# Kernel optimization log

Measured on AMD Instinct MI355X. Metric: run time of the kernel, lower is better.

The kernel has to match this reference:

```python
import jax, jax.numpy as jnp
import numpy as np

N, E, D, DE, H = 50000, 400000, 128, 64, 8
EPS = 1e-5
SLOPE = 0.2


def setup_inputs() -> dict:
    key = jax.random.key(0)
    ks = jax.random.split(key, 16)

    def lin(k, fan_in, fan_out):
        return (jax.random.normal(k, (fan_in, fan_out), jnp.float32) / np.sqrt(fan_in)).astype(jnp.float32)

    return {
        "node_features": jax.random.normal(ks[0], (N, D), jnp.float32),
        "edge_features": jax.random.normal(ks[1], (E, DE), jnp.float32),
        "Wn": lin(ks[2], D, D), "bn": jnp.zeros((D,), jnp.float32),
        "Wq": lin(ks[3], D, D), "bq": jnp.zeros((D,), jnp.float32),
        "Wk": lin(ks[4], D, D), "bk": jnp.zeros((D,), jnp.float32),
        "Wv": lin(ks[5], D, D), "bv": jnp.zeros((D,), jnp.float32),
        "We": lin(ks[6], DE, D), "be": jnp.zeros((D,), jnp.float32),
        "A1": lin(ks[7], 3 * D, D), "b1": jnp.zeros((D,), jnp.float32),
        "A2": lin(ks[8], D, H), "b2": jnp.zeros((H,), jnp.float32),
        "gamma": jnp.ones((D,), jnp.float32),
        "beta": jnp.zeros((D,), jnp.float32),
        "edge_index": jax.random.randint(ks[9], (2, E), 0, N, dtype=jnp.int32),
    }


def reference(node_features, edge_features, Wn, bn, Wq, bq, Wk, bk, Wv, bv,
              We, be, A1, b1, A2, b2, gamma, beta, edge_index):
    num_nodes = node_features.shape[0]
    h = node_features @ Wn + bn                      # [N, D]
    q = node_features @ Wq + bq                      # [N, D]
    k = node_features @ Wk + bk                      # [N, D]
    v = node_features @ Wv + bv                      # [N, D]
    eh = edge_features @ We + be                     # [E, D]

    src, tgt = edge_index[0], edge_index[1]
    attn_in = jnp.concatenate([q[src], k[tgt], eh], axis=-1)   # [E, 3D]
    hmid = jax.nn.leaky_relu(attn_in @ A1 + b1, SLOPE)          # [E, D]
    scores = jax.nn.leaky_relu(hmid @ A2 + b2, SLOPE)           # [E, H]
    w = jax.nn.softmax(scores.mean(axis=-1), axis=0)            # global softmax over edges, [E]

    # scatter-add: output[src] += w * v[tgt]
    out = jax.ops.segment_sum(w[:, None] * v[tgt], src, num_segments=num_nodes)  # [N, D]

    y = h + out                                       # dropout = identity (eval)
    mu = y.mean(axis=-1, keepdims=True)
    var = y.var(axis=-1, keepdims=True)
    return gamma * (y - mu) / jnp.sqrt(var + EPS) + beta
```

## Files before the change

kernel.cpp:

```cpp
#include <hip/hip_runtime.h>

#define D 128
#define DE 64
#define SLOPE 0.2f
#define EPS 1e-5f

typedef float f32x4 __attribute__((ext_vector_type(4)));
typedef short bf16x8 __attribute__((ext_vector_type(8)));
typedef unsigned short ushort;

__device__ __forceinline__ float lrelu(float x) { return x > 0.f ? x : SLOPE * x; }

__device__ __forceinline__ ushort f2bf(float x) {
  union { float f; unsigned u; } c; c.f = x;
  unsigned r = c.u + 0x7FFFu + ((c.u >> 16) & 1u);
  return (ushort)(r >> 16);
}
__device__ __forceinline__ float bf2f(unsigned u) {
  return __uint_as_float(u << 16);
}
__device__ __forceinline__ uint4 cvt8(const float* p) {
  float4 f0 = *(const float4*)p;
  float4 f1 = *(const float4*)(p + 4);
  union { ushort us[8]; uint4 v; } u;
  u.us[0] = f2bf(f0.x); u.us[1] = f2bf(f0.y);
  u.us[2] = f2bf(f0.z); u.us[3] = f2bf(f0.w);
  u.us[4] = f2bf(f1.x); u.us[5] = f2bf(f1.y);
  u.us[6] = f2bf(f1.z); u.us[7] = f2bf(f1.w);
  return u.v;
}

__global__ __launch_bounds__(128) void fold_pack(
    const float* __restrict__ Wq, const float* __restrict__ Wk,
    const float* __restrict__ We, const float* __restrict__ A1,
    const float* __restrict__ bq, const float* __restrict__ bk,
    const float* __restrict__ be, const float* __restrict__ b1,
    const float* __restrict__ Wn, const float* __restrict__ Wv,
    ushort* __restrict__ AfqP, ushort* __restrict__ AfkP,
    ushort* __restrict__ AfeP, float* __restrict__ bfold,
    ushort* __restrict__ WnP, ushort* __restrict__ WvP,
    const int* __restrict__ src, int* __restrict__ deg,
    int* __restrict__ rank, int E) {
  int r = blockIdx.x;
  int j = threadIdx.x;
  if (r < 128) {
    float acc = 0.f;
    for (int t = 0; t < 128; ++t) acc += Wq[r * 128 + t] * A1[t * 128 + j];
    int ch = r >> 5, quad = (r >> 3) & 3, jj = r & 7, nt = j >> 4, l15 = j & 15;
    AfqP[(((ch * 8 + nt) * 4 + quad) * 16 + l15) * 8 + jj] = f2bf(acc);
  } else if (r < 256) {
    int k = r - 128;
    float acc = 0.f;
    for (int t = 0; t < 128; ++t) acc += Wk[k * 128 + t] * A1[(128 + t) * 128 + j];
    int ch = k >> 5, quad = (k >> 3) & 3, jj = k & 7, nt = j >> 4, l15 = j & 15;
    AfkP[(((ch * 8 + nt) * 4 + quad) * 16 + l15) * 8 + jj] = f2bf(acc);
  } else if (r < 320) {
    int k = r - 256;
    float acc = 0.f;
    for (int t = 0; t < 128; ++t) acc += We[k * 128 + t] * A1[(256 + t) * 128 + j];
    int ch = k >> 5, quad = (k >> 3) & 3, jj = k & 7, nt = j >> 4, l15 = j & 15;
    AfeP[(((ch * 8 + nt) * 4 + quad) * 16 + l15) * 8 + jj] = f2bf(acc);
  } else if (r == 320) {
    float acc = b1[j];
    for (int t = 0; t < 128; ++t) {
      acc += bq[t] * A1[t * 128 + j];
      acc += bk[t] * A1[(128 + t) * 128 + j];
      acc += be[t] * A1[(256 + t) * 128 + j];
    }
    bfold[j] = acc;
  } else if (r < 449) {
    int c = r - 321;
    int ch = j >> 5, quad = (j >> 3) & 3, jj = j & 7, nt = c >> 4, l15 = c & 15;
    WnP[(((ch * 8 + nt) * 4 + quad) * 16 + l15) * 8 + jj] = f2bf(Wn[j * 128 + c]);
  } else if (r < 577) {
    int c = r - 449;
    int ch = j >> 5, quad = (j >> 3) & 3, jj = j & 7, nt = c >> 4, l15 = c & 15;
    WvP[(((ch * 8 + nt) * 4 + quad) * 16 + l15) * 8 + jj] = f2bf(Wv[j * 128 + c]);
  } else {
    int i = (r - 577) * 128 + j;
    if (i < E) rank[i] = atomicAdd(&deg[src[i]], 1);
  }
}

__global__ __launch_bounds__(256, 2) void node_gemm_mfma(
    const float* __restrict__ X, const ushort* __restrict__ WnP,
    const ushort* __restrict__ WvP, const ushort* __restrict__ AfqP,
    const ushort* __restrict__ AfkP, const float* __restrict__ bn,
    const float* __restrict__ bv, float* __restrict__ h,
    ushort* __restrict__ vb, ushort* __restrict__ q2p,
    ushort* __restrict__ k2p, int Nn) {
  __shared__ ushort As[128 * 40];
  __shared__ float bS[128];
  const ushort* BP;
  const float* bb = nullptr;
  float* O = nullptr;
  ushort* Ob = nullptr;
  int mode;
  switch (blockIdx.y) {
    case 0: BP = WnP; bb = bn; O = h; mode = 0; break;
    case 1: BP = WvP; bb = bv; Ob = vb; mode = 1; break;
    case 2: BP = AfqP; Ob = q2p; mode = 2; break;
    default: BP = AfkP; Ob = k2p; mode = 2; break;
  }
  const int t = threadIdx.x;
  if (t < 128) bS[t] = bb ? bb[t] : 0.f;
  const int seg = t & 3, arow = t >> 2;
  const int m0 = blockIdx.x * 128;
  int rIdx[2];
#pragma unroll
  for (int l = 0; l < 2; ++l) rIdx[l] = min(m0 + arow + 64 * l, Nn - 1);
  uint4 avA[2];
#pragma unroll
  for (int l = 0; l < 2; ++l)
    avA[l] = cvt8(X + (size_t)rIdx[l] * 128 + seg * 8);
  f32x4 acc[2][8];
#pragma unroll
  for (int mt = 0; mt < 2; ++mt)
#pragma unroll
    for (int nt = 0; nt < 8; ++nt) acc[mt][nt] = (f32x4)(0.f);
  const int lane = t & 63, wv = t >> 6, l15 = lane & 15, quad = lane >> 4;
  for (int ch = 0; ch < 4; ++ch) {
#pragma unroll
    for (int l = 0; l < 2; ++l)
      *(uint4*)&As[(arow + 64 * l) * 40 + seg * 8] = avA[l];
    __syncthreads();
    if (ch < 3) {
      int o = (ch + 1) * 32 + seg * 8;
#pragma unroll
      for (int l = 0; l < 2; ++l)
        avA[l] = cvt8(X + (size_t)rIdx[l] * 128 + o);
    }
    bf16x8 af[2];
#pragma unroll
    for (int mt = 0; mt < 2; ++mt)
      af[mt] = *(const bf16x8*)&As[(wv * 32 + mt * 16 + l15) * 40 + quad * 8];
    const ushort* bp = BP + ((size_t)(ch * 8) * 64 + lane) * 8;
#pragma unroll
    for (int nt = 0; nt < 8; ++nt) {
      bf16x8 bfr = *(const bf16x8*)(bp + nt * 512);
#pragma unroll
      for (int mt = 0; mt < 2; ++mt)
        acc[mt][nt] =
            __builtin_amdgcn_mfma_f32_16x16x32_bf16(af[mt], bfr, acc[mt][nt], 0, 0, 0);
    }
    __syncthreads();
  }
#pragma unroll
  for (int mt = 0; mt < 2; ++mt) {
    int rowb = m0 + wv * 32 + mt * 16 + quad * 4;
#pragma unroll
    for (int nt = 0; nt < 8; ++nt) {
      int col = nt * 16 + l15;
      float b = bS[col];
#pragma unroll
      for (int r = 0; r < 4; ++r) {
        int rg = rowb + r;
        if (rg < Nn) {
          if (mode == 0)      O[(size_t)rg * 128 + col] = acc[mt][nt][r] + b;
          else if (mode == 1) Ob[(size_t)rg * 128 + col] = f2bf(acc[mt][nt][r] + b);
          else                Ob[(size_t)rg * 128 + l15 * 8 + nt] = f2bf(acc[mt][nt][r]);
        }
      }
    }
  }
}

__global__ __launch_bounds__(256, 3) void edge_fused4(
    const float* __restrict__ EF, const ushort* __restrict__ AfeP,
    const float* __restrict__ bfold, const float* __restrict__ A2,
    const float* __restrict__ b2, const ushort* __restrict__ q2p,
    const ushort* __restrict__ k2p, const int* __restrict__ src,
    const int* __restrict__ tgt, const int* __restrict__ offs,
    const int* __restrict__ rank,
    int2* __restrict__ cwt, float2* __restrict__ part, int E) {
  __shared__ ushort As[128 * 40];
  __shared__ float A2s[8 * 128];
  __shared__ float bfS[128];
  __shared__ float b2s[8];
  __shared__ int sIdxS[128], sIdxT[128], sRank[128];
  __shared__ float redM[16], redS[16];
  const int t = threadIdx.x;
  const int e0 = blockIdx.x * 128;
  if (t < 128) {
    int ec = min(e0 + t, E - 1);
    sIdxS[t] = src[ec];
    sRank[t] = rank[ec];
    bfS[t] = bfold[t];
  } else {
    sIdxT[t - 128] = tgt[min(e0 + t - 128, E - 1)];
  }
  if (t < 8) b2s[t] = b2[t];
#pragma unroll
  for (int l = 0; l < 4; ++l) {
    int i = t + l * 256;
    A2s[(i & 7) * 128 + (i >> 3)] = A2[i];
  }
  const int seg = t & 3, arow = t >> 2;
  int ecl[2];
#pragma unroll
  for (int l = 0; l < 2; ++l) ecl[l] = min(e0 + arow + 64 * l, E - 1);
  uint4 avA[2];
#pragma unroll
  for (int l = 0; l < 2; ++l)
    avA[l] = cvt8(EF + (size_t)ecl[l] * 64 + seg * 8);
  f32x4 acc[2][8];
#pragma unroll
  for (int mt = 0; mt < 2; ++mt)
#pragma unroll
    for (int nt = 0; nt < 8; ++nt) acc[mt][nt] = (f32x4)(0.f);
  const int lane = t & 63, wv = t >> 6, l15 = lane & 15, quad = lane >> 4;

#pragma unroll
  for (int ch = 0; ch < 2; ++ch) {
#pragma unroll
    for (int l = 0; l < 2; ++l)
      *(uint4*)&As[(arow + 64 * l) * 40 + seg * 8] = avA[l];
    __syncthreads();
    if (ch == 0) {
      int o = 32 + seg * 8;
#pragma unroll
      for (int l = 0; l < 2; ++l)
        avA[l] = cvt8(EF + (size_t)ecl[l] * 64 + o);
    }
    bf16x8 af[2];
#pragma unroll
    for (int mt = 0; mt < 2; ++mt)
      af[mt] = *(const bf16x8*)&As[(wv * 32 + mt * 16 + l15) * 40 + quad * 8];
    const ushort* bp = AfeP + ((size_t)(ch * 8) * 64 + lane) * 8;
#pragma unroll
    for (int nt = 0; nt < 8; ++nt) {
      bf16x8 bfr = *(const bf16x8*)(bp + nt * 512);
#pragma unroll
      for (int mt = 0; mt < 2; ++mt)
        acc[mt][nt] =
            __builtin_amdgcn_mfma_f32_16x16x32_bf16(af[mt], bfr, acc[mt][nt], 0, 0, 0);
    }
    if (ch == 0) __syncthreads();
  }

  float bfv[8];
#pragma unroll
  for (int nt = 0; nt < 8; ++nt) bfv[nt] = bfS[nt * 16 + l15];
#pragma unroll
  for (int mt = 0; mt < 2; ++mt) {
#pragma unroll
    for (int r = 0; r < 4; ++r) {
      int erow = wv * 32 + mt * 16 + quad * 4 + r;
      int si = sIdxS[erow], ti = sIdxT[erow];
      uint4 qv = *(const uint4*)(q2p + (size_t)si * 128 + l15 * 8);
      uint4 kv = *(const uint4*)(k2p + (size_t)ti * 128 + l15 * 8);
      const ushort* qs = (const ushort*)&qv;
      const ushort* ks = (const ushort*)&kv;
#pragma unroll
      for (int nt = 0; nt < 8; ++nt)
        acc[mt][nt][r] =
            lrelu(acc[mt][nt][r] + bf2f(qs[nt]) + bf2f(ks[nt]) + bfv[nt]);
    }
  }
  float tacc[2][4];
#pragma unroll
  for (int mt = 0; mt < 2; ++mt)
#pragma unroll
    for (int r = 0; r < 4; ++r) tacc[mt][r] = 0.f;
  for (int hh = 0; hh < 8; ++hh) {
    float a2v[8];
#pragma unroll
    for (int nt = 0; nt < 8; ++nt) a2v[nt] = A2s[hh * 128 + nt * 16 + l15];
    float b2h = b2s[hh];
#pragma unroll
    for (int mt = 0; mt < 2; ++mt)
#pragma unroll
      for (int r = 0; r < 4; ++r) {
        float p = 0.f;
#pragma unroll
        for (int nt = 0; nt < 8; ++nt) p += acc[mt][nt][r] * a2v[nt];
        p += __shfl_xor(p, 1);
        p += __shfl_xor(p, 2);
        p += __shfl_xor(p, 4);
        p += __shfl_xor(p, 8);
        tacc[mt][r] += lrelu(p + b2h);
      }
  }
  if (l15 == 0) {
    float sc[8];
    float m = -1e30f;
#pragma unroll
    for (int mt = 0; mt < 2; ++mt)
#pragma unroll
      for (int r = 0; r < 4; ++r) {
        int i = mt * 4 + r;
        sc[i] = tacc[mt][r] * 0.125f;
        int e = e0 + wv * 32 + mt * 16 + quad * 4 + r;
        if (e < E) m = fmaxf(m, sc[i]);
      }
    float ssum = 0.f;
#pragma unroll
    for (int mt = 0; mt < 2; ++mt)
#pragma unroll
      for (int r = 0; r < 4; ++r) {
        int i = mt * 4 + r;
        int erow = wv * 32 + mt * 16 + quad * 4 + r;
        if (e0 + erow < E) {
          ssum += __expf(sc[i] - m);
          int j = offs[sIdxS[erow]] + sRank[erow];
          cwt[j] = make_int2(sIdxT[erow], __float_as_int(sc[i]));
        }
      }
    int rid = wv * 4 + quad;
    redM[rid] = m;
    redS[rid] = ssum;
  }
  __syncthreads();
  if (t == 0) {
    float M = redM[0], S = redS[0];
#pragma unroll
    for (int i = 1; i < 16; ++i) {
      float m2 = redM[i], s2 = redS[i];
      float Mn = fmaxf(M, m2);
      S = S * __expf(M - Mn) + s2 * __expf(m2 - Mn);
      M = Mn;
    }
    part[blockIdx.x] = make_float2(M, S);
  }
}

__global__ __launch_bounds__(256) void softmax_final(
    const float2* __restrict__ part, int nPart, float* __restrict__ MS) {
  __shared__ float mS[256], sS[256];
  int tid = threadIdx.x;
  float m = -1e30f, sum = 0.f;
  for (int i = tid; i < nPart; i += 256) {
    float2 p = part[i];
    float M = fmaxf(m, p.x);
    sum = sum * __expf(m - M) + p.y * __expf(p.x - M);
    m = M;
  }
  mS[tid] = m;
  sS[tid] = sum;
  __syncthreads();
  for (int off = 128; off > 0; off >>= 1) {
    if (tid < off) {
      float m1 = mS[tid], s1 = sS[tid];
      float m2 = mS[tid + off], s2 = sS[tid + off];
      float M = fmaxf(m1, m2);
      mS[tid] = M;
      sS[tid] = s1 * __expf(m1 - M) + s2 * __expf(m2 - M);
    }
    __syncthreads();
  }
  if (tid == 0) {
    MS[0] = mS[0];
    MS[1] = 1.f / sS[0];
  }
}

__global__ __launch_bounds__(256) void scan1(const int* __restrict__ deg,
                                             int* __restrict__ incl,
                                             int* __restrict__ bsum, int N) {
  __shared__ int sh[256];
  int tid = threadIdx.x;
  int i = blockIdx.x * 256 + tid;
  sh[tid] = (i < N) ? deg[i] : 0;
  __syncthreads();
  for (int off = 1; off < 256; off <<= 1) {
    int tv = (tid >= off) ? sh[tid - off] : 0;
    __syncthreads();
    sh[tid] += tv;
    __syncthreads();
  }
  if (i < N) incl[i] = sh[tid];
  if (tid == 255) bsum[blockIdx.x] = sh[255];
}

__global__ __launch_bounds__(256) void scan2(int* __restrict__ bsum, int nb) {
  __shared__ int sh[256];
  int tid = threadIdx.x;
  sh[tid] = (tid < nb) ? bsum[tid] : 0;
  __syncthreads();
  for (int off = 1; off < 256; off <<= 1) {
    int tv = (tid >= off) ? sh[tid - off] : 0;
    __syncthreads();
    sh[tid] += tv;
    __syncthreads();
  }
  if (tid < nb) bsum[tid] = sh[tid];
}

__global__ __launch_bounds__(256) void scan3(const int* __restrict__ deg,
                                             const int* __restrict__ incl,
                                             const int* __restrict__ bsum,
                                             int* __restrict__ offs, int N,
                                             int E) {
  int i = blockIdx.x * 256 + threadIdx.x;
  if (i >= N) return;
  int base = (blockIdx.x > 0) ? bsum[blockIdx.x - 1] : 0;
  int ex = incl[i] - deg[i] + base;
  offs[i] = ex;
  if (i == N - 1) offs[N] = E;
}

__global__ __launch_bounds__(256) void gather_ln(
    const int* __restrict__ offs, const int2* __restrict__ cwt,
    const ushort* __restrict__ vb, const float* __restrict__ MS,
    const float* __restrict__ gamma, const float* __restrict__ beta,
    float* __restrict__ y, int N) {
  int tid = threadIdx.x;
  int n = blockIdx.x * 4 + (tid >> 6);
  if (n >= N) return;
  int lane = tid & 63;
  float M = MS[0], inv = MS[1];
  int beg = offs[n], end = offs[n + 1];
  float a0 = 0.f, a1 = 0.f;
  int j = beg;
  for (; j + 4 <= end; j += 4) {
    int2 p0 = cwt[j], p1 = cwt[j + 1], p2 = cwt[j + 2], p3 = cwt[j + 3];
    unsigned u0 = *(const unsigned*)(vb + (size_t)p0.x * 128 + lane * 2);
    unsigned u1 = *(const unsigned*)(vb + (size_t)p1.x * 128 + lane * 2);
    unsigned u2 = *(const unsigned*)(vb + (size_t)p2.x * 128 + lane * 2);
    unsigned u3 = *(const unsigned*)(vb + (size_t)p3.x * 128 + lane * 2);
    float w0 = __expf(__int_as_float(p0.y) - M) * inv;
    float w1 = __expf(__int_as_float(p1.y) - M) * inv;
    float w2 = __expf(__int_as_float(p2.y) - M) * inv;
    float w3 = __expf(__int_as_float(p3.y) - M) * inv;
    a0 += w0 * bf2f(u0 & 0xffffu) + w1 * bf2f(u1 & 0xffffu) +
          w2 * bf2f(u2 & 0xffffu) + w3 * bf2f(u3 & 0xffffu);
    a1 += w0 * bf2f(u0 >> 16) + w1 * bf2f(u1 >> 16) + w2 * bf2f(u2 >> 16) +
          w3 * bf2f(u3 >> 16);
  }
  for (; j < end; ++j) {
    int2 p = cwt[j];
    float w = __expf(__int_as_float(p.y) - M) * inv;
    unsigned u = *(const unsigned*)(vb + (size_t)p.x * 128 + lane * 2);
    a0 += w * bf2f(u & 0xffffu);
    a1 += w * bf2f(u >> 16);
  }
  size_t base = (size_t)n * 128 + lane * 2;
  float2 hv = *(const float2*)(y + base);
  float y0 = hv.x + a0, y1 = hv.y + a1;
  float sum = y0 + y1, ssq = y0 * y0 + y1 * y1;
#pragma unroll
  for (int off = 1; off < 64; off <<= 1) {
    sum += __shfl_xor(sum, off);
    ssq += __shfl_xor(ssq, off);
  }
  float mu = sum * (1.f / 128.f);
  float var = ssq * (1.f / 128.f) - mu * mu;
  float rstd = rsqrtf(var + EPS);
  float2 g = *(const float2*)(gamma + lane * 2);
  float2 bt = *(const float2*)(beta + lane * 2);
  float2 out;
  out.x = g.x * (y0 - mu) * rstd + bt.x;
  out.y = g.y * (y1 - mu) * rstd + bt.y;
  *(float2*)(y + base) = out;
}

extern "C" void kernel_launch(void* const* d_in, const int* in_sizes, int n_in,
                              void* d_out, int out_size, void* d_ws,
                              size_t ws_size, hipStream_t stream) {
  const float* X  = (const float*)d_in[0];
  const float* EF = (const float*)d_in[1];
  const float* Wn = (const float*)d_in[2];
  const float* bn = (const float*)d_in[3];
  const float* Wq = (const float*)d_in[4];
  const float* bq = (const float*)d_in[5];
  const float* Wk = (const float*)d_in[6];
  const float* bk = (const float*)d_in[7];
  const float* Wv = (const float*)d_in[8];
  const float* bv = (const float*)d_in[9];
  const float* We = (const float*)d_in[10];
  const float* be = (const float*)d_in[11];
  const float* A1 = (const float*)d_in[12];
  const float* b1 = (const float*)d_in[13];
  const float* A2 = (const float*)d_in[14];
  const float* b2 = (const float*)d_in[15];
  const float* gamma = (const float*)d_in[16];
  const float* beta  = (const float*)d_in[17];
  const int* ei = (const int*)d_in[18];

  int N = in_sizes[0] / D;
  int E = in_sizes[1] / DE;
  const int* src = ei;
  const int* tgt = ei + E;

  float* h = (float*)d_out;
  float* ws = (float*)d_ws;
  float2* part = (float2*)ws;
  float* MS    = (float*)(part + 4096);
  float* bfold = MS + 4;
  ushort* vb   = (ushort*)(bfold + 128);
  ushort* q2p  = vb + (size_t)N * D;
  ushort* k2p  = q2p + (size_t)N * D;
  ushort* AfqP = k2p + (size_t)N * D;
  ushort* AfkP = AfqP + 128 * 128;
  ushort* AfeP = AfkP + 128 * 128;
  ushort* WnP  = AfeP + 128 * 64;
  ushort* WvP  = WnP + 128 * 128;
  int* deg    = (int*)(WvP + 128 * 128);
  int* incl   = deg + N;
  int* bsum   = incl + N;
  int* rank   = bsum + 256;
  int* offs   = rank + E;
  int2* cwt   = (int2*)(offs + N + 2);

  int nbScan = (N + 255) / 256;
  int nbEdge = (E + 127) / 128;
  int nbHist = (E + 127) / 128;

  hipMemsetAsync(deg, 0, (size_t)N * sizeof(int), stream);
  fold_pack<<<577 + nbHist, 128, 0, stream>>>(Wq, Wk, We, A1, bq, bk, be, b1,
                                              Wn, Wv, AfqP, AfkP, AfeP, bfold,
                                              WnP, WvP, src, deg, rank, E);
  scan1<<<nbScan, 256, 0, stream>>>(deg, incl, bsum, N);
  scan2<<<1, 256, 0, stream>>>(bsum, nbScan);
  scan3<<<nbScan, 256, 0, stream>>>(deg, incl, bsum, offs, N, E);
  node_gemm_mfma<<<dim3((N + 127) / 128, 4), 256, 0, stream>>>(
      X, WnP, WvP, AfqP, AfkP, bn, bv, h, vb, q2p, k2p, N);
  edge_fused4<<<nbEdge, 256, 0, stream>>>(EF, AfeP, bfold, A2, b2, q2p, k2p,
                                          src, tgt, offs, rank, cwt, part, E);
  softmax_final<<<1, 256, 0, stream>>>(part, nbEdge, MS);
  gather_ln<<<(N + 3) / 4, 256, 0, stream>>>(offs, cwt, vb, MS, gamma, beta, h,
                                             N);
}
```

Measured before the change: 369.7 us.

## Pre-convert node features to bf16 once and prefetch edge gathers early

Node features are converted to bf16 once inside the fold/pack kernel, so the node GEMM's four y-blocks read a half-size bf16 copy instead of each re-reading and converting the fp32 input. The edge kernel now stages both K-chunks of edge features into a wider shared tile with a single barrier. It also issues the q/k gather loads for the first row group before the MFMA loop so their latency overlaps compute. This costs an extra bf16 buffer write and read plus more shared memory per block in the edge kernel, which may reduce occupancy.

```diff
diff --git a/kernel.cpp b/kernel.cpp
--- a/kernel.cpp
+++ b/kernel.cpp
@@ -40,7 +40,8 @@
     ushort* __restrict__ AfeP, float* __restrict__ bfold,
     ushort* __restrict__ WnP, ushort* __restrict__ WvP,
     const int* __restrict__ src, int* __restrict__ deg,
-    int* __restrict__ rank, int E) {
+    int* __restrict__ rank, const float* __restrict__ X,
+    ushort* __restrict__ Xb, int Nn, int E) {
   int r = blockIdx.x;
   int j = threadIdx.x;
   if (r < 128) {
@@ -77,13 +78,21 @@
     int ch = j >> 5, quad = (j >> 3) & 3, jj = j & 7, nt = c >> 4, l15 = c & 15;
     WvP[(((ch * 8 + nt) * 4 + quad) * 16 + l15) * 8 + jj] = f2bf(Wv[j * 128 + c]);
   } else {
-    int i = (r - 577) * 128 + j;
-    if (i < E) rank[i] = atomicAdd(&deg[src[i]], 1);
+    int rr = r - 577;
+    int nbHist = (E + 127) >> 7;
+    if (rr < nbHist) {
+      int i = rr * 128 + j;
+      if (i < E) rank[i] = atomicAdd(&deg[src[i]], 1);
+    } else {
+      size_t base = (size_t)(rr - nbHist) * 1024 + (size_t)j * 8;
+      if (base < (size_t)Nn * 128)
+        *(uint4*)(Xb + base) = cvt8(X + base);
+    }
   }
 }
 
 __global__ __launch_bounds__(256, 2) void node_gemm_mfma(
-    const float* __restrict__ X, const ushort* __restrict__ WnP,
+    const ushort* __restrict__ Xb, const ushort* __restrict__ WnP,
     const ushort* __restrict__ WvP, const ushort* __restrict__ AfqP,
     const ushort* __restrict__ AfkP, const float* __restrict__ bn,
     const float* __restrict__ bv, float* __restrict__ h,
@@ -112,7 +121,7 @@
   uint4 avA[2];
 #pragma unroll
   for (int l = 0; l < 2; ++l)
-    avA[l] = cvt8(X + (size_t)rIdx[l] * 128 + seg * 8);
+    avA[l] = *(const uint4*)(Xb + (size_t)rIdx[l] * 128 + seg * 8);
   f32x4 acc[2][8];
 #pragma unroll
   for (int mt = 0; mt < 2; ++mt)
@@ -128,7 +137,7 @@
       int o = (ch + 1) * 32 + seg * 8;
 #pragma unroll
       for (int l = 0; l < 2; ++l)
-        avA[l] = cvt8(X + (size_t)rIdx[l] * 128 + o);
+        avA[l] = *(const uint4*)(Xb + (size_t)rIdx[l] * 128 + o);
     }
     bf16x8 af[2];
 #pragma unroll
@@ -173,7 +182,7 @@
     const int* __restrict__ tgt, const int* __restrict__ offs,
     const int* __restrict__ rank,
     int2* __restrict__ cwt, float2* __restrict__ part, int E) {
-  __shared__ ushort As[128 * 40];
+  __shared__ ushort As[128 * 88];
   __shared__ float A2s[8 * 128];
   __shared__ float bfS[128];
   __shared__ float b2s[8];
@@ -199,62 +208,73 @@
   int ecl[2];
 #pragma unroll
   for (int l = 0; l < 2; ++l) ecl[l] = min(e0 + arow + 64 * l, E - 1);
-  uint4 avA[2];
-#pragma unroll
-  for (int l = 0; l < 2; ++l)
-    avA[l] = cvt8(EF + (size_t)ecl[l] * 64 + seg * 8);
+  const int lane = t & 63, wv = t >> 6, l15 = lane & 15, quad = lane >> 4;
+  {
+    uint4 a0 = cvt8(EF + (size_t)ecl[0] * 64 + seg * 8);
+    uint4 a1 = cvt8(EF + (size_t)ecl[1] * 64 + seg * 8);
+    uint4 a2 = cvt8(EF + (size_t)ecl[0] * 64 + 32 + seg * 8);
+    uint4 a3 = cvt8(EF + (size_t)ecl[1] * 64 + 32 + seg * 8);
+    *(uint4*)&As[arow * 88 + seg * 8] = a0;
+    *(uint4*)&As[(arow + 64) * 88 + seg * 8] = a1;
+    *(uint4*)&As[arow * 88 + 48 + seg * 8] = a2;
+    *(uint4*)&As[(arow + 64) * 88 + 48 + seg * 8] = a3;
+  }
   f32x4 acc[2][8];
 #pragma unroll
   for (int mt = 0; mt < 2; ++mt)
 #pragma unroll
     for (int nt = 0; nt < 8; ++nt) acc[mt][nt] = (f32x4)(0.f);
-  const int lane = t & 63, wv = t >> 6, l15 = lane & 15, quad = lane >> 4;
-
+  __syncthreads();
+
+  const int er0 = wv * 32 + quad * 4;
+  uint4 qv0[4], kv0[4];
+#pragma unroll
+  for (int r = 0; r < 4; ++r) {
+    qv0[r] = *(const uint4*)(q2p + (size_t)sIdxS[er0 + r] * 128 + l15 * 8);
+    kv0[r] = *(const uint4*)(k2p + (size_t)sIdxT[er0 + r] * 128 + l15 * 8);
+  }
 #pragma unroll
   for (int ch = 0; ch < 2; ++ch) {
-#pragma unroll
-    for (int l = 0; l < 2; ++l)
-      *(uint4*)&As[(arow + 64 * l) * 40 + seg * 8] = avA[l];
-    __syncthreads();
-    if (ch == 0) {
-      int o = 32 + seg * 8;
-#pragma unroll
-      for (int l = 0; l < 2; ++l)
-        avA[l] = cvt8(EF + (size_t)ecl[l] * 64 + o);
-    }
-    bf16x8 af[2];
-#pragma unroll
-    for (int mt = 0; mt < 2; ++mt)
-      af[mt] = *(const bf16x8*)&As[(wv * 32 + mt * 16 + l15) * 40 + quad * 8];
+    bf16x8 af0 = *(const bf16x8*)&As[(wv * 32 + l15) * 88 + ch * 48 + quad * 8];
+    bf16x8 af1 =
+        *(const bf16x8*)&As[(wv * 32 + 16 + l15) * 88 + ch * 48 + quad * 8];
     const ushort* bp = AfeP + ((size_t)(ch * 8) * 64 + lane) * 8;
 #pragma unroll
     for (int nt = 0; nt < 8; ++nt) {
       bf16x8 bfr = *(const bf16x8*)(bp + nt * 512);
-#pragma unroll
-      for (int mt = 0; mt < 2; ++mt)
-        acc[mt][nt] =
-            __builtin_amdgcn_mfma_f32_16x16x32_bf16(af[mt], bfr, acc[mt][nt], 0, 0, 0);
-    }
-    if (ch == 0) __syncthreads();
+      acc[0][nt] = __builtin_amdgcn_mfma_f32_16x16x32_bf16(af0, bfr, acc[0][nt], 0, 0, 0);
+      acc[1][nt] = __builtin_amdgcn_mfma_f32_16x16x32_bf16(af1, bfr, acc[1][nt], 0, 0, 0);
+    }
   }
 
   float bfv[8];
 #pragma unroll
   for (int nt = 0; nt < 8; ++nt) bfv[nt] = bfS[nt * 16 + l15];
 #pragma unroll
-  for (int mt = 0; mt < 2; ++mt) {
+  for (int r = 0; r < 4; ++r) {
+    const ushort* qs = (const ushort*)&qv0[r];
+    const ushort* ks = (const ushort*)&kv0[r];
+#pragma unroll
+    for (int nt = 0; nt < 8; ++nt)
+      acc[0][nt][r] =
+          lrelu(acc[0][nt][r] + bf2f(qs[nt]) + bf2f(ks[nt]) + bfv[nt]);
+  }
+  {
+    const int er1 = er0 + 16;
+    uint4 qv1[4], kv1[4];
 #pragma unroll
     for (int r = 0; r < 4; ++r) {
-      int erow = wv * 32 + mt * 16 + quad * 4 + r;
-      int si = sIdxS[erow], ti = sIdxT[erow];
-      uint4 qv = *(const uint4*)(q2p + (size_t)si * 128 + l15 * 8);
-      uint4 kv = *(const uint4*)(k2p + (size_t)ti * 128 + l15 * 8);
-      const ushort* qs = (const ushort*)&qv;
-      const ushort* ks = (const ushort*)&kv;
+      qv1[r] = *(const uint4*)(q2p + (size_t)sIdxS[er1 + r] * 128 + l15 * 8);
+      kv1[r] = *(const uint4*)(k2p + (size_t)sIdxT[er1 + r] * 128 + l15 * 8);
+    }
+#pragma unroll
+    for (int r = 0; r < 4; ++r) {
+      const ushort* qs = (const ushort*)&qv1[r];
+      const ushort* ks = (const ushort*)&kv1[r];
 #pragma unroll
       for (int nt = 0; nt < 8; ++nt)
-        acc[mt][nt][r] =
-            lrelu(acc[mt][nt][r] + bf2f(qs[nt]) + bf2f(ks[nt]) + bfv[nt]);
+        acc[1][nt][r] =
+            lrelu(acc[1][nt][r] + bf2f(qs[nt]) + bf2f(ks[nt]) + bfv[nt]);
     }
   }
   float tacc[2][4];
@@ -501,20 +521,22 @@
   int* rank   = bsum + 256;
   int* offs   = rank + E;
   int2* cwt   = (int2*)(offs + N + 2);
+  ushort* Xb  = (ushort*)(cwt + E);
 
   int nbScan = (N + 255) / 256;
   int nbEdge = (E + 127) / 128;
   int nbHist = (E + 127) / 128;
+  int nbXb   = (N * 128 + 1023) / 1024;
 
   hipMemsetAsync(deg, 0, (size_t)N * sizeof(int), stream);
-  fold_pack<<<577 + nbHist, 128, 0, stream>>>(Wq, Wk, We, A1, bq, bk, be, b1,
-                                              Wn, Wv, AfqP, AfkP, AfeP, bfold,
-                                              WnP, WvP, src, deg, rank, E);
+  fold_pack<<<577 + nbHist + nbXb, 128, 0, stream>>>(
+      Wq, Wk, We, A1, bq, bk, be, b1, Wn, Wv, AfqP, AfkP, AfeP, bfold, WnP,
+      WvP, src, deg, rank, X, Xb, N, E);
   scan1<<<nbScan, 256, 0, stream>>>(deg, incl, bsum, N);
   scan2<<<1, 256, 0, stream>>>(bsum, nbScan);
   scan3<<<nbScan, 256, 0, stream>>>(deg, incl, bsum, offs, N, E);
   node_gemm_mfma<<<dim3((N + 127) / 128, 4), 256, 0, stream>>>(
-      X, WnP, WvP, AfqP, AfkP, bn, bv, h, vb, q2p, k2p, N);
+      Xb, WnP, WvP, AfqP, AfkP, bn, bv, h, vb, q2p, k2p, N);
   edge_fused4<<<nbEdge, 256, 0, stream>>>(EF, AfeP, bfold, A2, b2, q2p, k2p,
                                           src, tgt, offs, rank, cwt, part, E);
   softmax_final<<<1, 256, 0, stream>>>(part, nbEdge, MS);
```

After: 378.1 us. 1.02x slower.
